# Performance work log

Hardware: AMD Instinct MI355X
Metric: run time of the kernel (lower is better)

Reference implementation:

```python
import jax, jax.numpy as jnp
import numpy as np


def setup_inputs() -> dict:
    key = jax.random.key(0)
    ks = jax.random.split(key, 8)
    B, N, D, E = 8, 64, 64, 32
    nodes = jax.random.normal(ks[0], (B, N, D), dtype=jnp.float32)
    edges = jax.random.normal(ks[1], (B, N * N, E), dtype=jnp.float32)
    mask = jax.random.uniform(ks[2], (B, N * N, 1), dtype=jnp.float32)
    W_e = jax.random.normal(ks[3], (E, D * D), dtype=jnp.float32) * 0.05
    b_e = jnp.zeros((D * D,), dtype=jnp.float32)
    gru_kernel = jax.random.normal(ks[4], (D, 3 * D), dtype=jnp.float32) * 0.05
    gru_rkernel = jax.random.normal(ks[5], (D, 3 * D), dtype=jnp.float32) * 0.05
    gru_bias = jnp.zeros((2, 3 * D), dtype=jnp.float32)
    return {"nodes": nodes, "edges": edges, "mask": mask, "W_e": W_e,
            "b_e": b_e, "gru_kernel": gru_kernel, "gru_rkernel": gru_rkernel,
            "gru_bias": gru_bias}


def _gru_step(x, h, K, R, bias):
    # keras GRU with reset_after=True
    D = h.shape[-1]
    xk = x @ K + bias[0]          # [M, 3D]
    hk = h @ R + bias[1]          # [M, 3D]
    xz, xr, xh = xk[:, :D], xk[:, D:2 * D], xk[:, 2 * D:]
    hz, hr, hh_ = hk[:, :D], hk[:, D:2 * D], hk[:, 2 * D:]
    z = jax.nn.sigmoid(xz + hz)
    r = jax.nn.sigmoid(xr + hr)
    hh = jnp.tanh(xh + r * hh_)
    return z * h + (1.0 - z) * hh


def reference(nodes, edges, mask, W_e, b_e, gru_kernel, gru_rkernel, gru_bias):
    B, N, D = nodes.shape
    # edge-conditioned transform matrices: [B, N*N, D, D]
    A = jax.nn.relu(edges @ W_e + b_e).reshape(B, N * N, D, D)
    # state_j = tile(nodes, [1, N, 1]) -> [B, N*N, D]
    state_j = jnp.tile(nodes, (1, N, 1))
    # per-edge small matmul A @ node_j
    messages = jnp.einsum('beij,bej->bei', A, state_j)  # [B, N*N, D]
    masked = (messages * mask).reshape(B, N, N, D)
    agg = masked.sum(axis=2)  # [B, N, D]
    # GRU over length-2 sequence [old_state, agg_messages], batch B*N, h0=0
    h = jnp.zeros((B * N, D), dtype=nodes.dtype)
    h = _gru_step(nodes.reshape(B * N, D), h, gru_kernel, gru_rkernel, gru_bias)
    h = _gru_step(agg.reshape(B * N, D), h, gru_kernel, gru_rkernel, gru_bias)
    return h.reshape(B, N, D)
```

## Files before the change

kernel.cpp:

```cpp
#include <hip/hip_runtime.h>

typedef _Float16 half8 __attribute__((ext_vector_type(8)));
typedef float floatx4 __attribute__((ext_vector_type(4)));
typedef float floatx2 __attribute__((ext_vector_type(2)));

#define BB 8
#define NN 64
#define DD 64
#define EE 32

__global__ void prep_w_kernel(const float* __restrict__ W_e,
                              _Float16* __restrict__ WT) {
    const int d  = blockIdx.x * 64 + (threadIdx.x & 63);
    const int kq = threadIdx.x >> 6;
    half8 buf;
#pragma unroll
    for (int j = 0; j < 8; ++j)
        buf[j] = (_Float16)W_e[(kq * 8 + j) * 4096 + d];
    *reinterpret_cast<half8*>(WT + d * 32 + kq * 8) = buf;
}

__device__ __forceinline__ floatx2 relu2(floatx2 v) {
    floatx2 z = {0.f, 0.f};
    return __builtin_elementwise_max(v, z);
}
__device__ __forceinline__ float sigmoidf_(float x) { return 1.f / (1.f + __expf(-x)); }
__device__ __forceinline__ float tanhf_(float x) {
    float e = __expf(2.f * x);
    return (e - 1.f) / (e + 1.f);
}

__global__ __launch_bounds__(256, 2)
void fused_kernel(const _Float16* __restrict__ WT,
                  const float* __restrict__ edges,
                  const float* __restrict__ nodes,
                  const float* __restrict__ mask,
                  const float* __restrict__ b_e,
                  const float* __restrict__ K,
                  const float* __restrict__ R,
                  const float* __restrict__ bias,
                  float* __restrict__ out) {
    const int b     = blockIdx.x >> 6;
    const int inode = blockIdx.x & 63;
    const int tid   = threadIdx.x;
    const int w     = tid >> 6;
    const int lane  = tid & 63;
    const int quad  = lane >> 4;
    const int col   = lane & 15;
    const int row   = b * 64 + inode;

    __shared__ float S[4][64][17];
    __shared__ float P[4][64];
    __shared__ float xs[64], aggs[64], h1s[64];
    __shared__ float g1[192], g2[192];

    if (tid < 64) xs[tid] = nodes[row * 64 + tid];

    half8 ef[4];
#pragma unroll
    for (int eb = 0; eb < 4; ++eb) {
        const float* ep = edges + (b * 4096 + inode * 64 + eb * 16 + col) * 32 + quad * 8;
        floatx4 e0 = *reinterpret_cast<const floatx4*>(ep);
        floatx4 e1 = *reinterpret_cast<const floatx4*>(ep + 4);
#pragma unroll
        for (int j = 0; j < 4; ++j) {
            ef[eb][j]     = (_Float16)e0[j];
            ef[eb][4 + j] = (_Float16)e1[j];
        }
    }

    floatx2 xm[4][2];
#pragma unroll
    for (int eb = 0; eb < 4; ++eb) {
        int j = eb * 16 + col;
        float mk = mask[b * 4096 + inode * 64 + j];
#pragma unroll
        for (int r = 0; r < 4; ++r) {
            int jj = w * 16 + quad * 4 + r;
            xm[eb][r >> 1][r & 1] = mk * nodes[(b * 64 + j) * 64 + jj];
        }
    }

    const _Float16* aptr = WT + (w * 16 + col) * 32 + quad * 8;
    const float*    bptr = b_e + w * 16 + quad * 4;

    half8   af = *reinterpret_cast<const half8*>(aptr);
    floatx4 bf = *reinterpret_cast<const floatx4*>(bptr);

    for (int i = 0; i < 64; ++i) {
        int inx = (i + 1) & 63;
        half8   af_n = *reinterpret_cast<const half8*>(aptr + inx * 64 * 32);
        floatx4 bf_n = *reinterpret_cast<const floatx4*>(bptr + inx * 64);

        floatx4 c[4];
        c[0] = __builtin_amdgcn_mfma_f32_16x16x32_f16(af, ef[0], bf, 0, 0, 0);
        c[1] = __builtin_amdgcn_mfma_f32_16x16x32_f16(af, ef[1], bf, 0, 0, 0);
        c[2] = __builtin_amdgcn_mfma_f32_16x16x32_f16(af, ef[2], bf, 0, 0, 0);
        c[3] = __builtin_amdgcn_mfma_f32_16x16x32_f16(af, ef[3], bf, 0, 0, 0);

        floatx2 sv = {0.f, 0.f};
#pragma unroll
        for (int eb = 0; eb < 4; ++eb) {
            floatx2* cp = reinterpret_cast<floatx2*>(&c[eb]);
            sv += relu2(cp[0]) * xm[eb][0];
            sv += relu2(cp[1]) * xm[eb][1];
        }
        float s = sv[0] + sv[1];
        s += __shfl_xor(s, 32);
        s += __shfl_xor(s, 16);
        if (lane < 16) S[w][i][lane] = s;

        af = af_n; bf = bf_n;
    }
    __syncthreads();

    {
        int ii = tid & 63, ww = tid >> 6;
        float p = 0.f;
#pragma unroll
        for (int l = 0; l < 16; ++l) p += S[ww][ii][l];
        P[ww][ii] = p;
    }
    __syncthreads();
    if (tid < 64) aggs[tid] = P[0][tid] + P[1][tid] + P[2][tid] + P[3][tid];
    __syncthreads();

    if (tid < 192) {
        float acc = bias[tid];
#pragma unroll 4
        for (int k = 0; k < 64; ++k) acc = fmaf(xs[k], K[k * 192 + tid], acc);
        g1[tid] = acc;
    }
    __syncthreads();
    if (tid < 64) {
        float z  = sigmoidf_(g1[tid]       + bias[192 + tid]);
        float r  = sigmoidf_(g1[64 + tid]  + bias[256 + tid]);
        float hh = tanhf_  (g1[128 + tid] + r * bias[320 + tid]);
        h1s[tid] = (1.f - z) * hh;
    }
    __syncthreads();

    if (tid < 192) {
        float a1 = bias[tid], a2 = bias[192 + tid];
#pragma unroll 4
        for (int k = 0; k < 64; ++k) {
            a1 = fmaf(aggs[k], K[k * 192 + tid], a1);
            a2 = fmaf(h1s[k],  R[k * 192 + tid], a2);
        }
        g1[tid] = a1; g2[tid] = a2;
    }
    __syncthreads();
    if (tid < 64) {
        float z  = sigmoidf_(g1[tid]       + g2[tid]);
        float r  = sigmoidf_(g1[64 + tid]  + g2[64 + tid]);
        float hh = tanhf_  (g1[128 + tid] + r * g2[128 + tid]);
        out[row * 64 + tid] = z * h1s[tid] + (1.f - z) * hh;
    }
}

extern "C" void kernel_launch(void* const* d_in, const int* in_sizes, int n_in,
                              void* d_out, int out_size, void* d_ws, size_t ws_size,
                              hipStream_t stream) {
    const float* nodes = (const float*)d_in[0];
    const float* edges = (const float*)d_in[1];
    const float* mask  = (const float*)d_in[2];
    const float* W_e   = (const float*)d_in[3];
    const float* b_e   = (const float*)d_in[4];
    const float* gk    = (const float*)d_in[5];
    const float* gr    = (const float*)d_in[6];
    const float* gb    = (const float*)d_in[7];
    float* out = (float*)d_out;

    _Float16* WT = (_Float16*)d_ws;

    prep_w_kernel<<<64, 256, 0, stream>>>(W_e, WT);
    fused_kernel<<<512, 256, 0, stream>>>(WT, edges, nodes, mask, b_e, gk, gr, gb, out);
}
```

Measured before the change: 99.96 us.

## Fold weight prep into fused kernel with grid flag and overlap GRU step

```diff
diff --git a/kernel.cpp b/kernel.cpp
--- a/kernel.cpp
+++ b/kernel.cpp
@@ -9,29 +9,18 @@
 #define DD 64
 #define EE 32
 
-__global__ void prep_w_kernel(const float* __restrict__ W_e,
-                              _Float16* __restrict__ WT) {
-    const int d  = blockIdx.x * 64 + (threadIdx.x & 63);
-    const int kq = threadIdx.x >> 6;
-    half8 buf;
-#pragma unroll
-    for (int j = 0; j < 8; ++j)
-        buf[j] = (_Float16)W_e[(kq * 8 + j) * 4096 + d];
-    *reinterpret_cast<half8*>(WT + d * 32 + kq * 8) = buf;
-}
-
-__device__ __forceinline__ floatx2 relu2(floatx2 v) {
-    floatx2 z = {0.f, 0.f};
-    return __builtin_elementwise_max(v, z);
-}
 __device__ __forceinline__ float sigmoidf_(float x) { return 1.f / (1.f + __expf(-x)); }
 __device__ __forceinline__ float tanhf_(float x) {
     float e = __expf(2.f * x);
     return (e - 1.f) / (e + 1.f);
 }
+__device__ __forceinline__ floatx2 relu2(floatx2 v) {
+    floatx2 z = {0.f, 0.f};
+    return __builtin_elementwise_max(v, z);
+}
 
 __global__ __launch_bounds__(256, 2)
-void fused_kernel(const _Float16* __restrict__ WT,
+void fused_kernel(const float* __restrict__ W_e,
                   const float* __restrict__ edges,
                   const float* __restrict__ nodes,
                   const float* __restrict__ mask,
@@ -39,9 +28,12 @@
                   const float* __restrict__ K,
                   const float* __restrict__ R,
                   const float* __restrict__ bias,
+                  _Float16* __restrict__ WT,
+                  int* __restrict__ flag,
                   float* __restrict__ out) {
-    const int b     = blockIdx.x >> 6;
-    const int inode = blockIdx.x & 63;
+    const int bid   = blockIdx.x;
+    const int b     = bid >> 6;
+    const int inode = bid & 63;
     const int tid   = threadIdx.x;
     const int w     = tid >> 6;
     const int lane  = tid & 63;
@@ -53,6 +45,19 @@
     __shared__ float P[4][64];
     __shared__ float xs[64], aggs[64], h1s[64];
     __shared__ float g1[192], g2[192];
+
+    if (bid < 64) {
+        const int d  = bid * 64 + (tid & 63);
+        const int kq = tid >> 6;
+        half8 buf;
+#pragma unroll
+        for (int j = 0; j < 8; ++j)
+            buf[j] = (_Float16)W_e[(kq * 8 + j) * 4096 + d];
+        *reinterpret_cast<half8*>(WT + d * 32 + kq * 8) = buf;
+        __syncthreads();
+        if (tid == 0)
+            __hip_atomic_fetch_add(flag, 1, __ATOMIC_RELEASE, __HIP_MEMORY_SCOPE_AGENT);
+    }
 
     if (tid < 64) xs[tid] = nodes[row * 64 + tid];
 
@@ -81,22 +86,44 @@
         }
     }
 
+    __syncthreads();
+    if (tid < 192) {
+        float acc = bias[tid];
+#pragma unroll 8
+        for (int k = 0; k < 64; ++k) acc = fmaf(xs[k], K[k * 192 + tid], acc);
+        g1[tid] = acc;
+    }
+    __syncthreads();
+    if (tid < 64) {
+        float z  = sigmoidf_(g1[tid]       + bias[192 + tid]);
+        float r  = sigmoidf_(g1[64 + tid]  + bias[256 + tid]);
+        float hh = tanhf_  (g1[128 + tid] + r * bias[320 + tid]);
+        h1s[tid] = (1.f - z) * hh;
+    }
+
+    if (tid == 0) {
+        while (__hip_atomic_load(flag, __ATOMIC_ACQUIRE, __HIP_MEMORY_SCOPE_AGENT) < 64) {}
+    }
+    __syncthreads();
+
     const _Float16* aptr = WT + (w * 16 + col) * 32 + quad * 8;
     const float*    bptr = b_e + w * 16 + quad * 4;
 
-    half8   af = *reinterpret_cast<const half8*>(aptr);
-    floatx4 bf = *reinterpret_cast<const floatx4*>(bptr);
+    half8   af0 = *reinterpret_cast<const half8*>(aptr);
+    floatx4 bf0 = *reinterpret_cast<const floatx4*>(bptr);
+    half8   af1 = *reinterpret_cast<const half8*>(aptr + 2048);
+    floatx4 bf1 = *reinterpret_cast<const floatx4*>(bptr + 64);
 
     for (int i = 0; i < 64; ++i) {
-        int inx = (i + 1) & 63;
-        half8   af_n = *reinterpret_cast<const half8*>(aptr + inx * 64 * 32);
-        floatx4 bf_n = *reinterpret_cast<const floatx4*>(bptr + inx * 64);
+        int ip2 = (i + 2) & 63;
+        half8   afn = *reinterpret_cast<const half8*>(aptr + ip2 * 2048);
+        floatx4 bfn = *reinterpret_cast<const floatx4*>(bptr + ip2 * 64);
 
         floatx4 c[4];
-        c[0] = __builtin_amdgcn_mfma_f32_16x16x32_f16(af, ef[0], bf, 0, 0, 0);
-        c[1] = __builtin_amdgcn_mfma_f32_16x16x32_f16(af, ef[1], bf, 0, 0, 0);
-        c[2] = __builtin_amdgcn_mfma_f32_16x16x32_f16(af, ef[2], bf, 0, 0, 0);
-        c[3] = __builtin_amdgcn_mfma_f32_16x16x32_f16(af, ef[3], bf, 0, 0, 0);
+        c[0] = __builtin_amdgcn_mfma_f32_16x16x32_f16(af0, ef[0], bf0, 0, 0, 0);
+        c[1] = __builtin_amdgcn_mfma_f32_16x16x32_f16(af0, ef[1], bf0, 0, 0, 0);
+        c[2] = __builtin_amdgcn_mfma_f32_16x16x32_f16(af0, ef[2], bf0, 0, 0, 0);
+        c[3] = __builtin_amdgcn_mfma_f32_16x16x32_f16(af0, ef[3], bf0, 0, 0, 0);
 
         floatx2 sv = {0.f, 0.f};
 #pragma unroll
@@ -110,7 +137,7 @@
         s += __shfl_xor(s, 16);
         if (lane < 16) S[w][i][lane] = s;
 
-        af = af_n; bf = bf_n;
+        af0 = af1; bf0 = bf1; af1 = afn; bf1 = bfn;
     }
     __syncthreads();
 
@@ -126,23 +153,8 @@
     __syncthreads();
 
     if (tid < 192) {
-        float acc = bias[tid];
-#pragma unroll 4
-        for (int k = 0; k < 64; ++k) acc = fmaf(xs[k], K[k * 192 + tid], acc);
-        g1[tid] = acc;
-    }
-    __syncthreads();
-    if (tid < 64) {
-        float z  = sigmoidf_(g1[tid]       + bias[192 + tid]);
-        float r  = sigmoidf_(g1[64 + tid]  + bias[256 + tid]);
-        float hh = tanhf_  (g1[128 + tid] + r * bias[320 + tid]);
-        h1s[tid] = (1.f - z) * hh;
-    }
-    __syncthreads();
-
-    if (tid < 192) {
         float a1 = bias[tid], a2 = bias[192 + tid];
-#pragma unroll 4
+#pragma unroll 8
         for (int k = 0; k < 64; ++k) {
             a1 = fmaf(aggs[k], K[k * 192 + tid], a1);
             a2 = fmaf(h1s[k],  R[k * 192 + tid], a2);
@@ -171,8 +183,11 @@
     const float* gb    = (const float*)d_in[7];
     float* out = (float*)d_out;
 
-    _Float16* WT = (_Float16*)d_ws;
+    char* ws = (char*)d_ws;
+    int*      flag = (int*)ws;
+    _Float16* WT   = (_Float16*)(ws + 256);
 
-    prep_w_kernel<<<64, 256, 0, stream>>>(W_e, WT);
-    fused_kernel<<<512, 256, 0, stream>>>(WT, edges, nodes, mask, b_e, gk, gr, gb, out);
+    hipMemsetAsync(flag, 0, sizeof(int), stream);
+    fused_kernel<<<512, 256, 0, stream>>>(W_e, edges, nodes, mask, b_e,
+                                          gk, gr, gb, WT, flag, out);
 }
```

After: 101.8 us. No clear change (+1.9%).
